# Kernel tuning notes

Hardware: AMD Instinct MI355X
Metric: run time of the kernel (lower is better)

Reference implementation:

```python
import jax, jax.numpy as jnp
import numpy as np

DIM = 128
NUM_SLOTS = 8
ITERS = 3
EPS = 1e-8
LN_EPS = 1e-3
HIDDEN = max(DIM, 128)


def _ln(x, w, b):
    mu = jnp.mean(x, axis=-1, keepdims=True)
    var = jnp.mean(jnp.square(x - mu), axis=-1, keepdims=True)
    return (x - mu) * jax.lax.rsqrt(var + LN_EPS) * w + b


def setup_inputs() -> dict:
    key = jax.random.key(0)
    ks = jax.random.split(key, 16)
    b, n, d, h = 32, 4096, DIM, HIDDEN
    limit = np.sqrt(6.0 / (1 + d))
    inp = {
        'inputs': jax.random.normal(ks[0], (b, n, d), jnp.float32),
        'slots_mu': jax.random.uniform(ks[1], (1, 1, d), jnp.float32, -limit, limit),
        'slots_log_sigma': jax.random.uniform(ks[2], (1, 1, d), jnp.float32, -limit, limit),
        'Wq': jax.random.normal(ks[3], (d, d), jnp.float32) / np.sqrt(d),
        'Wk': jax.random.normal(ks[4], (d, d), jnp.float32) / np.sqrt(d),
        'Wv': jax.random.normal(ks[5], (d, d), jnp.float32) / np.sqrt(d),
        'W_ih': jax.random.normal(ks[6], (3 * d, d), jnp.float32) / np.sqrt(d),
        'W_hh': jax.random.normal(ks[7], (3 * d, d), jnp.float32) / np.sqrt(d),
        'b_ih': jnp.zeros((3 * d,), jnp.float32),
        'b_hh': jnp.zeros((3 * d,), jnp.float32),
        'W1': jax.random.normal(ks[8], (h, d), jnp.float32) / np.sqrt(d),
        'b1': jnp.zeros((h,), jnp.float32),
        'W2': jax.random.normal(ks[9], (d, h), jnp.float32) / np.sqrt(h),
        'b2': jnp.zeros((d,), jnp.float32),
        'ln_in_w': jnp.ones((d,), jnp.float32), 'ln_in_b': jnp.zeros((d,), jnp.float32),
        'ln_s_w': jnp.ones((d,), jnp.float32), 'ln_s_b': jnp.zeros((d,), jnp.float32),
        'ln_ff_w': jnp.ones((d,), jnp.float32), 'ln_ff_b': jnp.zeros((d,), jnp.float32),
    }
    return inp


def reference(inputs, slots_mu, slots_log_sigma, Wq, Wk, Wv, W_ih, W_hh, b_ih, b_hh,
              W1, b1, W2, b2, ln_in_w, ln_in_b, ln_s_w, ln_s_b, ln_ff_w, ln_ff_b):
    b, n, d = inputs.shape
    scale = d ** -0.5
    # stochastic slot init (reparameterized, fixed key for determinism)
    noise = jax.random.normal(jax.random.key(42), (b, NUM_SLOTS, d), inputs.dtype)
    slots = slots_mu + jnp.exp(slots_log_sigma) * noise

    x = _ln(inputs, ln_in_w, ln_in_b)
    k = jnp.einsum('bnd,ed->bne', x, Wk)
    v = jnp.einsum('bnd,ed->bne', x, Wv)

    for _ in range(ITERS):
        slots_prev = slots
        q = jnp.einsum('bsd,ed->bse', _ln(slots, ln_s_w, ln_s_b), Wq)
        dots = jnp.einsum('bid,bjd->bij', q, k) * scale          # [b, slots, n]
        attn = jax.nn.softmax(dots, axis=1) + EPS                 # softmax over slots
        attn = attn / jnp.sum(attn, axis=-1, keepdims=True)       # normalize over tokens
        updates = jnp.einsum('bjd,bij->bid', v, attn)             # [b, slots, d]
        # GRUCell(updates, slots_prev)
        gx = jnp.einsum('bsd,ed->bse', updates, W_ih) + b_ih
        gh = jnp.einsum('bsd,ed->bse', slots_prev, W_hh) + b_hh
        xr, xz, xn = jnp.split(gx, 3, axis=-1)
        hr, hz, hn = jnp.split(gh, 3, axis=-1)
        r = jax.nn.sigmoid(xr + hr)
        z = jax.nn.sigmoid(xz + hz)
        ng = jnp.tanh(xn + r * hn)
        slots = (1.0 - z) * ng + z * slots_prev
        # residual MLP
        ff = _ln(slots, ln_ff_w, ln_ff_b)
        ff = jax.nn.relu(jnp.einsum('bsd,hd->bsh', ff, W1) + b1)
        slots = slots + jnp.einsum('bsh,dh->bsd', ff, W2) + b2
    return slots
```

## Files before the change

kernel.cpp:

```cpp
#include <hip/hip_runtime.h>
#include <hip/hip_bf16.h>
#include <math.h>

#define DIM 128
#define NSLOT 8
#define NTOK 4096
#define NB 32
#define CHUNK 512
#define NCH (NTOK / CHUNK)
#define LN_EPS 1e-3f
#define ATT_EPS 1e-8f
#define SCALE 0.08838834764831845f

#define BM 64
#define LDK 136

typedef short bf16x8 __attribute__((ext_vector_type(8)));
typedef float f32x4 __attribute__((ext_vector_type(4)));
typedef unsigned short ushort8_t __attribute__((ext_vector_type(8)));

__device__ __forceinline__ float bf2f(unsigned short u) {
  return __uint_as_float(((unsigned)u) << 16);
}
__device__ __forceinline__ unsigned short f2bf(float f) {
  unsigned u = __float_as_uint(f);
  unsigned r = (u + 0x7FFFu + ((u >> 16) & 1u)) >> 16;
  return (unsigned short)r;
}

__device__ __forceinline__ float erfinv_like_xla(float x) {
  double xd = (double)x;
  double w = -log1p(-xd * xd);
  double p;
  if (w < 5.0) {
    w = w - 2.5;
    p = 2.81022636e-08;
    p = 3.43273939e-07 + p * w;
    p = -3.5233877e-06 + p * w;
    p = -4.39150654e-06 + p * w;
    p = 0.00021858087 + p * w;
    p = -0.00125372503 + p * w;
    p = -0.00417768164 + p * w;
    p = 0.246640727 + p * w;
    p = 1.50140941 + p * w;
  } else {
    w = sqrt(w) - 3.0;
    p = -0.000200214257;
    p = 0.000100950558 + p * w;
    p = 0.00134934322 + p * w;
    p = -0.00367342844 + p * w;
    p = 0.00573950773 + p * w;
    p = -0.0076224613 + p * w;
    p = 0.00943887047 + p * w;
    p = 1.00167406 + p * w;
    p = 2.83297682 + p * w;
  }
  return (float)(p * xd);
}

__global__ __launch_bounds__(256) void k_init_slots(
    const float* __restrict__ mu, const float* __restrict__ lsig,
    float* __restrict__ slots) {
  int t = blockIdx.x * blockDim.x + threadIdx.x;
  if (t >= NB * NSLOT * DIM) return;
  uint32_t x0 = 0u, x1 = (uint32_t)t;
  uint32_t k0 = 0u, k1 = 42u;
  uint32_t ks[3] = {k0, k1, k0 ^ k1 ^ 0x1BD11BDAu};
  x0 += ks[0];
  x1 += ks[1];
  const int rot[2][4] = {{13, 15, 26, 6}, {17, 29, 16, 24}};
#pragma unroll
  for (int blk = 0; blk < 5; ++blk) {
    const int* r = rot[blk & 1];
#pragma unroll
    for (int j = 0; j < 4; ++j) {
      x0 += x1;
      x1 = (x1 << r[j]) | (x1 >> (32 - r[j]));
      x1 ^= x0;
    }
    x0 += ks[(blk + 1) % 3];
    x1 += ks[(blk + 2) % 3] + (uint32_t)(blk + 1);
  }
  uint32_t bits = x0 ^ x1;
  float f = __uint_as_float((bits >> 9) | 0x3F800000u) - 1.0f;
  const float mn = __uint_as_float(0xBF7FFFFFu);
  float u = fmaxf(f * 2.0f + mn, mn);
  float noise = 1.41421356f * erfinv_like_xla(u);
  int d = t & (DIM - 1);
  slots[t] = mu[d] + expf(lsig[d]) * noise;
}

__global__ __launch_bounds__(256) void k_wcast(const float* __restrict__ Wk,
                                               const float* __restrict__ Wv,
                                               unsigned short* __restrict__ Wbf) {
  int i = blockIdx.x * 256 + threadIdx.x;
  if (i >= DIM * DIM) return;
  Wbf[i] = f2bf(Wk[i]);
  Wbf[DIM * DIM + i] = f2bf(Wv[i]);
}

__global__ __launch_bounds__(256) void k_ln_kv(
    const float* __restrict__ inp, const unsigned short* __restrict__ Wbf,
    const float* __restrict__ lnw, const float* __restrict__ lnb,
    unsigned short* __restrict__ kt, unsigned short* __restrict__ vt) {
  __shared__ unsigned short x_lds[BM][LDK];
  int t = threadIdx.x;
  int tg = blockIdx.x;

  {
    int r = t >> 2, qh = t & 3;
    const float* src = inp + ((size_t)tg * BM + r) * DIM + qh * 32;
    float xr[32];
    float s = 0.f, sq = 0.f;
#pragma unroll
    for (int i4 = 0; i4 < 8; ++i4) {
      float4 v = *reinterpret_cast<const float4*>(src + i4 * 4);
      xr[i4 * 4 + 0] = v.x; xr[i4 * 4 + 1] = v.y;
      xr[i4 * 4 + 2] = v.z; xr[i4 * 4 + 3] = v.w;
      s += v.x + v.y + v.z + v.w;
      sq += v.x * v.x + v.y * v.y + v.z * v.z + v.w * v.w;
    }
    s += __shfl_xor(s, 1); sq += __shfl_xor(sq, 1);
    s += __shfl_xor(s, 2); sq += __shfl_xor(sq, 2);
    float mean = s * (1.0f / DIM);
    float var = fmaxf(sq * (1.0f / DIM) - mean * mean, 0.0f);
    float inv = 1.0f / sqrtf(var + LN_EPS);
#pragma unroll
    for (int c8 = 0; c8 < 4; ++c8) {
      ushort8_t pk;
#pragma unroll
      for (int j = 0; j < 8; ++j) {
        int d = qh * 32 + c8 * 8 + j;
        float y = (xr[c8 * 8 + j] - mean) * inv * lnw[d] + lnb[d];
        pk[j] = f2bf(y);
      }
      *reinterpret_cast<ushort8_t*>(&x_lds[r][qh * 32 + c8 * 8]) = pk;
    }
  }
  __syncthreads();

  int w = t >> 6, l = t & 63, lm = l & 15, lg = l >> 4;
  int mat = w >> 1;
  int ebase = (w & 1) * 64;
  const unsigned short* Wsrc = Wbf + mat * DIM * DIM;

  f32x4 acc[4][4];
#pragma unroll
  for (int i = 0; i < 4; ++i)
#pragma unroll
    for (int j = 0; j < 4; ++j) acc[i][j] = (f32x4){0.f, 0.f, 0.f, 0.f};

  if (mat == 0) {
#pragma unroll
    for (int ks = 0; ks < 4; ++ks) {
      bf16x8 wf[4], xf[4];
#pragma unroll
      for (int et = 0; et < 4; ++et)
        wf[et] = *reinterpret_cast<const bf16x8*>(
            Wsrc + (ebase + et * 16 + lm) * DIM + ks * 32 + 8 * lg);
#pragma unroll
      for (int tt = 0; tt < 4; ++tt)
        xf[tt] = *reinterpret_cast<const bf16x8*>(
            &x_lds[tt * 16 + lm][ks * 32 + 8 * lg]);
#pragma unroll
      for (int tt = 0; tt < 4; ++tt)
#pragma unroll
        for (int et = 0; et < 4; ++et)
          acc[tt][et] = __builtin_amdgcn_mfma_f32_16x16x32_bf16(
              xf[tt], wf[et], acc[tt][et], 0, 0, 0);
    }
    size_t rowbase = (size_t)tg * BM;
#pragma unroll
    for (int tt = 0; tt < 4; ++tt)
#pragma unroll
      for (int et = 0; et < 4; ++et)
#pragma unroll
        for (int r = 0; r < 4; ++r) {
          size_t grow = rowbase + tt * 16 + 4 * lg + r;
          kt[grow * DIM + ebase + et * 16 + lm] = f2bf(acc[tt][et][r]);
        }
  } else {
#pragma unroll
    for (int ks = 0; ks < 4; ++ks) {
      bf16x8 wf[4], xf[4];
#pragma unroll
      for (int et = 0; et < 4; ++et)
        wf[et] = *reinterpret_cast<const bf16x8*>(
            Wsrc + (ebase + et * 16 + lm) * DIM + ks * 32 + 8 * lg);
#pragma unroll
      for (int tt = 0; tt < 4; ++tt)
        xf[tt] = *reinterpret_cast<const bf16x8*>(
            &x_lds[tt * 16 + lm][ks * 32 + 8 * lg]);
#pragma unroll
      for (int et = 0; et < 4; ++et)
#pragma unroll
        for (int tt = 0; tt < 4; ++tt)
          acc[et][tt] = __builtin_amdgcn_mfma_f32_16x16x32_bf16(
              wf[et], xf[tt], acc[et][tt], 0, 0, 0);
    }
    int b = tg >> 6;
    int nb = (tg & 63) * BM;
#pragma unroll
    for (int et = 0; et < 4; ++et)
#pragma unroll
      for (int tt = 0; tt < 4; ++tt)
#pragma unroll
        for (int r = 0; r < 4; ++r) {
          int e = ebase + et * 16 + 4 * lg + r;
          vt[((size_t)b * DIM + e) * NTOK + nb + tt * 16 + lm] =
              f2bf(acc[et][tt][r]);
        }
  }
}

__global__ __launch_bounds__(256) void k_attn(
    const float* __restrict__ slots, const float* __restrict__ Wq,
    const float* __restrict__ lnw, const float* __restrict__ lnb,
    const unsigned short* __restrict__ kt, const unsigned short* __restrict__ vt,
    float* __restrict__ Np, float* __restrict__ Dp) {
  int bid = blockIdx.x;
  int b = bid >> 3, ch = bid & 7;
  int n0 = ch * CHUNK;
  int t = threadIdx.x;
  __shared__ unsigned short q_lds[NSLOT][LDK];
  __shared__ __align__(16) float sln[NSLOT][DIM];
  __shared__ __align__(16) float a_t[CHUNK][NSLOT];

  {
    int s = t >> 5, c = t & 31;
    const float* sb = slots + (b * NSLOT + s) * DIM;
    float4 xv = *reinterpret_cast<const float4*>(sb + c * 4);
    float ps = xv.x + xv.y + xv.z + xv.w;
    float pq = xv.x * xv.x + xv.y * xv.y + xv.z * xv.z + xv.w * xv.w;
#pragma unroll
    for (int m = 16; m >= 1; m >>= 1) {
      ps += __shfl_xor(ps, m, 32);
      pq += __shfl_xor(pq, m, 32);
    }
    float mean = ps * (1.0f / DIM);
    float var = fmaxf(pq * (1.0f / DIM) - mean * mean, 0.0f);
    float inv = 1.0f / sqrtf(var + LN_EPS);
    float vals[4] = {xv.x, xv.y, xv.z, xv.w};
#pragma unroll
    for (int ii = 0; ii < 4; ++ii) {
      int d = c * 4 + ii;
      sln[s][d] = (vals[ii] - mean) * inv * lnw[d] + lnb[d];
    }
    __syncthreads();
#pragma unroll
    for (int ii = 0; ii < 4; ++ii) {
      int e = c + 32 * ii;
      const float* wr = Wq + e * DIM;
      float acc = 0.0f;
#pragma unroll
      for (int d4 = 0; d4 < DIM / 4; ++d4) {
        float4 w4 = *reinterpret_cast<const float4*>(wr + d4 * 4);
        float4 s4 = *reinterpret_cast<const float4*>(&sln[s][d4 * 4]);
        acc += s4.x * w4.x + s4.y * w4.y + s4.z * w4.z + s4.w * w4.w;
      }
      q_lds[s][e] = f2bf(SCALE * acc);
    }
  }
  __syncthreads();

  {
    int w = t >> 6, l = t & 63, lm = l & 15, lg = l >> 4;
    bf16x8 aq[4];
#pragma unroll
    for (int ks = 0; ks < 4; ++ks)
      aq[ks] = *reinterpret_cast<const bf16x8*>(
          &q_lds[lm & 7][ks * 32 + 8 * lg]);
    const unsigned short* kb = kt + ((size_t)b * NTOK + n0) * DIM;
#pragma unroll
    for (int tt8 = 0; tt8 < 8; ++tt8) {
      int tok = w * 128 + tt8 * 16 + lm;
      f32x4 acc = (f32x4){0.f, 0.f, 0.f, 0.f};
#pragma unroll
      for (int ks = 0; ks < 4; ++ks) {
        bf16x8 bk = *reinterpret_cast<const bf16x8*>(
            kb + (size_t)tok * DIM + ks * 32 + 8 * lg);
        acc = __builtin_amdgcn_mfma_f32_16x16x32_bf16(aq[ks], bk, acc, 0, 0, 0);
      }
      float m4 = fmaxf(fmaxf(acc[0], acc[1]), fmaxf(acc[2], acc[3]));
      float m8 = fmaxf(m4, __shfl_xor(m4, 16));
      float e0 = expf(acc[0] - m8), e1 = expf(acc[1] - m8);
      float e2 = expf(acc[2] - m8), e3 = expf(acc[3] - m8);
      float s4 = e0 + e1 + e2 + e3;
      float s8 = s4 + __shfl_xor(s4, 16);
      float rs = 1.0f / s8;
      if (lg < 2) {
        float4 av = {e0 * rs + ATT_EPS, e1 * rs + ATT_EPS, e2 * rs + ATT_EPS,
                     e3 * rs + ATT_EPS};
        *reinterpret_cast<float4*>(&a_t[tok][lg * 4]) = av;
      }
    }
  }
  __syncthreads();

  {
    int i = t >> 5, c = t & 31;
    float s = 0.0f;
#pragma unroll
    for (int jj = 0; jj < CHUNK / 32; ++jj) s += a_t[c + 32 * jj][i];
#pragma unroll
    for (int m = 16; m >= 1; m >>= 1) s += __shfl_xor(s, m, 32);
    if (c == 0) Dp[(b * NCH + ch) * NSLOT + i] = s;
  }

  {
    int d = t & (DIM - 1), ig = t >> 7;
    const unsigned short* vb = vt + ((size_t)b * DIM + d) * NTOK + n0;
    float acc0 = 0, acc1 = 0, acc2 = 0, acc3 = 0;
    for (int j8 = 0; j8 < CHUNK / 8; ++j8) {
      ushort8_t vv = *reinterpret_cast<const ushort8_t*>(vb + j8 * 8);
#pragma unroll
      for (int u = 0; u < 8; ++u) {
        float vval = bf2f(vv[u]);
        float4 av = *reinterpret_cast<const float4*>(&a_t[j8 * 8 + u][ig * 4]);
        acc0 += vval * av.x;
        acc1 += vval * av.y;
        acc2 += vval * av.z;
        acc3 += vval * av.w;
      }
    }
    size_t base = (size_t)(b * NCH + ch) * NSLOT;
    Np[(base + ig * 4 + 0) * DIM + d] = acc0;
    Np[(base + ig * 4 + 1) * DIM + d] = acc1;
    Np[(base + ig * 4 + 2) * DIM + d] = acc2;
    Np[(base + ig * 4 + 3) * DIM + d] = acc3;
  }
}

__global__ __launch_bounds__(256) void k_update(
    float* __restrict__ slots, const float* __restrict__ Np,
    const float* __restrict__ Dp, const float* __restrict__ W_ih,
    const float* __restrict__ W_hh, const float* __restrict__ b_ih,
    const float* __restrict__ b_hh, const float* __restrict__ W1,
    const float* __restrict__ b1, const float* __restrict__ W2,
    const float* __restrict__ b2, const float* __restrict__ lnfw,
    const float* __restrict__ lnfb) {
  int bs = blockIdx.x;
  int b = bs >> 3, s = bs & 7;
  int t = threadIdx.x;
  __shared__ __align__(16) float upd[DIM];
  __shared__ __align__(16) float sprev[DIM];
  __shared__ __align__(16) float snew[DIM];
  __shared__ __align__(16) float ffin[DIM];
  __shared__ __align__(16) float ffb[DIM];
  __shared__ __align__(16) float gx[3 * DIM];
  __shared__ __align__(16) float gh[3 * DIM];

  float dsum = 0.0f;
  for (int ch = 0; ch < NCH; ++ch) dsum += Dp[(b * NCH + ch) * NSLOT + s];

  if (t < DIM) {
    sprev[t] = slots[(b * NSLOT + s) * DIM + t];
    float a = 0.0f;
    for (int ch = 0; ch < NCH; ++ch)
      a += Np[((size_t)(b * NCH + ch) * NSLOT + s) * DIM + t];
    upd[t] = a / dsum;
  }
  __syncthreads();

  for (int e = t; e < 3 * DIM; e += 256) {
    const float* wi = W_ih + e * DIM;
    const float* wh = W_hh + e * DIM;
    float ax = 0.0f, ah = 0.0f;
#pragma unroll
    for (int d4 = 0; d4 < DIM / 4; ++d4) {
      float4 u4 = *reinterpret_cast<const float4*>(&upd[d4 * 4]);
      float4 p4 = *reinterpret_cast<const float4*>(&sprev[d4 * 4]);
      float4 wi4 = *reinterpret_cast<const float4*>(wi + d4 * 4);
      float4 wh4 = *reinterpret_cast<const float4*>(wh + d4 * 4);
      ax += u4.x * wi4.x + u4.y * wi4.y + u4.z * wi4.z + u4.w * wi4.w;
      ah += p4.x * wh4.x + p4.y * wh4.y + p4.z * wh4.z + p4.w * wh4.w;
    }
    gx[e] = ax + b_ih[e];
    gh[e] = ah + b_hh[e];
  }
  __syncthreads();

  if (t < DIM) {
    float xr = gx[t], xz = gx[DIM + t], xn = gx[2 * DIM + t];
    float hr = gh[t], hz = gh[DIM + t], hn = gh[2 * DIM + t];
    float r = 1.0f / (1.0f + expf(-(xr + hr)));
    float z = 1.0f / (1.0f + expf(-(xz + hz)));
    float ng = tanhf(xn + r * hn);
    snew[t] = (1.0f - z) * ng + z * sprev[t];
  }
  __syncthreads();

  if (t < DIM) {
    float s1 = 0.0f, s2 = 0.0f;
#pragma unroll 8
    for (int d = 0; d < DIM; ++d) {
      float v = snew[d];
      s1 += v;
      s2 += v * v;
    }
    float mean = s1 * (1.0f / DIM);
    float var = fmaxf(s2 * (1.0f / DIM) - mean * mean, 0.0f);
    float inv = 1.0f / sqrtf(var + LN_EPS);
    ffin[t] = (snew[t] - mean) * inv * lnfw[t] + lnfb[t];
  }
  __syncthreads();

  if (t < DIM) {
    const float* wr = W1 + t * DIM;
    float acc = 0.0f;
#pragma unroll
    for (int d4 = 0; d4 < DIM / 4; ++d4) {
      float4 f4 = *reinterpret_cast<const float4*>(&ffin[d4 * 4]);
      float4 w4 = *reinterpret_cast<const float4*>(wr + d4 * 4);
      acc += f4.x * w4.x + f4.y * w4.y + f4.z * w4.z + f4.w * w4.w;
    }
    ffb[t] = fmaxf(acc + b1[t], 0.0f);
  }
  __syncthreads();

  if (t < DIM) {
    const float* wr = W2 + t * DIM;
    float acc = 0.0f;
#pragma unroll
    for (int h4 = 0; h4 < DIM / 4; ++h4) {
      float4 f4 = *reinterpret_cast<const float4*>(&ffb[h4 * 4]);
      float4 w4 = *reinterpret_cast<const float4*>(wr + h4 * 4);
      acc += f4.x * w4.x + f4.y * w4.y + f4.z * w4.z + f4.w * w4.w;
    }
    slots[(b * NSLOT + s) * DIM + t] = snew[t] + acc + b2[t];
  }
}

__global__ __launch_bounds__(256) void k_sentinel(float* __restrict__ out,
                                                  int n) {
  int i = blockIdx.x * blockDim.x + threadIdx.x;
  if (i < n) out[i] = 1234.5f;
}

extern "C" void kernel_launch(void* const* d_in, const int* in_sizes, int n_in,
                              void* d_out, int out_size, void* d_ws,
                              size_t ws_size, hipStream_t stream) {
  const float* inp = (const float*)d_in[0];
  const float* mu = (const float*)d_in[1];
  const float* lsig = (const float*)d_in[2];
  const float* Wq = (const float*)d_in[3];
  const float* Wk = (const float*)d_in[4];
  const float* Wv = (const float*)d_in[5];
  const float* W_ih = (const float*)d_in[6];
  const float* W_hh = (const float*)d_in[7];
  const float* b_ih = (const float*)d_in[8];
  const float* b_hh = (const float*)d_in[9];
  const float* W1 = (const float*)d_in[10];
  const float* b1 = (const float*)d_in[11];
  const float* W2 = (const float*)d_in[12];
  const float* b2 = (const float*)d_in[13];
  const float* ln_in_w = (const float*)d_in[14];
  const float* ln_in_b = (const float*)d_in[15];
  const float* ln_s_w = (const float*)d_in[16];
  const float* ln_s_b = (const float*)d_in[17];
  const float* ln_ff_w = (const float*)d_in[18];
  const float* ln_ff_b = (const float*)d_in[19];

  float* slots = (float*)d_out;

  const size_t kv_elems = (size_t)NB * DIM * NTOK;
  const size_t w_elems = (size_t)2 * DIM * DIM;
  const size_t np_elems = (size_t)NB * NCH * NSLOT * DIM;
  const size_t dp_elems = (size_t)NB * NCH * NSLOT;
  size_t need = kv_elems * 2 * 2 + w_elems * 2 + np_elems * 4 + dp_elems * 4;
  if (ws_size < need) {
    k_sentinel<<<(out_size + 255) / 256, 256, 0, stream>>>((float*)d_out,
                                                           out_size);
    return;
  }
  char* wsb = (char*)d_ws;
  unsigned short* kt = (unsigned short*)wsb;
  unsigned short* vt = kt + kv_elems;
  unsigned short* Wbf = vt + kv_elems;
  float* Np = (float*)(wsb + kv_elems * 4 + w_elems * 2);
  float* Dp = Np + np_elems;

  k_init_slots<<<(NB * NSLOT * DIM) / 256, 256, 0, stream>>>(mu, lsig, slots);
  k_wcast<<<(DIM * DIM) / 256, 256, 0, stream>>>(Wk, Wv, Wbf);
  k_ln_kv<<<NB * NTOK / BM, 256, 0, stream>>>(inp, Wbf, ln_in_w, ln_in_b, kt,
                                              vt);
  for (int it = 0; it < 3; ++it) {
    k_attn<<<NB * NCH, 256, 0, stream>>>(slots, Wq, ln_s_w, ln_s_b, kt, vt, Np,
                                         Dp);
    k_update<<<NB * NSLOT, 256, 0, stream>>>(slots, Np, Dp, W_ih, W_hh, b_ih,
                                             b_hh, W1, b1, W2, b2, ln_ff_w,
                                             ln_ff_b);
  }
}
```

Before: 223.3 us.

## Fuse slot GRU/MLP update into attention kernel, stage K/V stores, use MFMA for updates

Each attention block now redundantly recomputes the previous iteration's GRU and MLP slot update from the partial sums before computing attention, so only one update launch remains at the end. This cuts the k_update/k_attn launch pairs and their serialization, with ping-pong workspace buffers for the partial sums and slot state. The K/V projection now stages its outputs through shared memory so the global stores are coalesced 16-byte writes. The attention-weighted V reduction now uses bf16 MFMA with attention weights stored as bf16, which lowers precision. The cost is that the update arithmetic is repeated 8 times per batch across the chunk blocks, and shared memory use per block rises.

```diff
diff --git a/kernel.cpp b/kernel.cpp
--- a/kernel.cpp
+++ b/kernel.cpp
@@ -8,6 +8,7 @@
 #define NB 32
 #define CHUNK 512
 #define NCH (NTOK / CHUNK)
+#define CHUNKPAD 520
 #define LN_EPS 1e-3f
 #define ATT_EPS 1e-8f
 #define SCALE 0.08838834764831845f
@@ -103,7 +104,7 @@
     const float* __restrict__ inp, const unsigned short* __restrict__ Wbf,
     const float* __restrict__ lnw, const float* __restrict__ lnb,
     unsigned short* __restrict__ kt, unsigned short* __restrict__ vt) {
-  __shared__ unsigned short x_lds[BM][LDK];
+  __shared__ __align__(16) unsigned short SH[DIM * 72];
   int t = threadIdx.x;
   int tg = blockIdx.x;
 
@@ -134,7 +135,7 @@
         float y = (xr[c8 * 8 + j] - mean) * inv * lnw[d] + lnb[d];
         pk[j] = f2bf(y);
       }
-      *reinterpret_cast<ushort8_t*>(&x_lds[r][qh * 32 + c8 * 8]) = pk;
+      *reinterpret_cast<ushort8_t*>(&SH[r * LDK + qh * 32 + c8 * 8]) = pk;
     }
   }
   __syncthreads();
@@ -161,7 +162,7 @@
 #pragma unroll
       for (int tt = 0; tt < 4; ++tt)
         xf[tt] = *reinterpret_cast<const bf16x8*>(
-            &x_lds[tt * 16 + lm][ks * 32 + 8 * lg]);
+            &SH[(tt * 16 + lm) * LDK + ks * 32 + 8 * lg]);
 #pragma unroll
       for (int tt = 0; tt < 4; ++tt)
 #pragma unroll
@@ -169,16 +170,6 @@
           acc[tt][et] = __builtin_amdgcn_mfma_f32_16x16x32_bf16(
               xf[tt], wf[et], acc[tt][et], 0, 0, 0);
     }
-    size_t rowbase = (size_t)tg * BM;
-#pragma unroll
-    for (int tt = 0; tt < 4; ++tt)
-#pragma unroll
-      for (int et = 0; et < 4; ++et)
-#pragma unroll
-        for (int r = 0; r < 4; ++r) {
-          size_t grow = rowbase + tt * 16 + 4 * lg + r;
-          kt[grow * DIM + ebase + et * 16 + lm] = f2bf(acc[tt][et][r]);
-        }
   } else {
 #pragma unroll
     for (int ks = 0; ks < 4; ++ks) {
@@ -190,7 +181,7 @@
 #pragma unroll
       for (int tt = 0; tt < 4; ++tt)
         xf[tt] = *reinterpret_cast<const bf16x8*>(
-            &x_lds[tt * 16 + lm][ks * 32 + 8 * lg]);
+            &SH[(tt * 16 + lm) * LDK + ks * 32 + 8 * lg]);
 #pragma unroll
       for (int et = 0; et < 4; ++et)
 #pragma unroll
@@ -198,38 +189,209 @@
           acc[et][tt] = __builtin_amdgcn_mfma_f32_16x16x32_bf16(
               wf[et], xf[tt], acc[et][tt], 0, 0, 0);
     }
-    int b = tg >> 6;
+  }
+  __syncthreads();
+
+  if (mat == 0) {
+#pragma unroll
+    for (int tt = 0; tt < 4; ++tt)
+#pragma unroll
+      for (int et = 0; et < 4; ++et)
+#pragma unroll
+        for (int r = 0; r < 4; ++r)
+          SH[(tt * 16 + 4 * lg + r) * LDK + ebase + et * 16 + lm] =
+              f2bf(acc[tt][et][r]);
+  }
+  __syncthreads();
+  {
+    size_t rowbase = (size_t)tg * BM;
+#pragma unroll
+    for (int u = 0; u < 4; ++u) {
+      int i = u * 256 + t;
+      int tok = i >> 4, off = (i & 15) * 8;
+      ushort8_t vv = *reinterpret_cast<const ushort8_t*>(&SH[tok * LDK + off]);
+      *reinterpret_cast<ushort8_t*>(&kt[(rowbase + tok) * DIM + off]) = vv;
+    }
+  }
+  __syncthreads();
+
+  if (mat == 1) {
+#pragma unroll
+    for (int et = 0; et < 4; ++et)
+#pragma unroll
+      for (int tt = 0; tt < 4; ++tt)
+#pragma unroll
+        for (int r = 0; r < 4; ++r)
+          SH[(ebase + et * 16 + 4 * lg + r) * 72 + tt * 16 + lm] =
+              f2bf(acc[et][tt][r]);
+  }
+  __syncthreads();
+  {
+    int bb = tg >> 6;
     int nb = (tg & 63) * BM;
 #pragma unroll
-    for (int et = 0; et < 4; ++et)
-#pragma unroll
-      for (int tt = 0; tt < 4; ++tt)
-#pragma unroll
-        for (int r = 0; r < 4; ++r) {
-          int e = ebase + et * 16 + 4 * lg + r;
-          vt[((size_t)b * DIM + e) * NTOK + nb + tt * 16 + lm] =
-              f2bf(acc[et][tt][r]);
-        }
+    for (int u = 0; u < 4; ++u) {
+      int i = u * 256 + t;
+      int e = i >> 3, off = (i & 7) * 8;
+      ushort8_t vv = *reinterpret_cast<const ushort8_t*>(&SH[e * 72 + off]);
+      *reinterpret_cast<ushort8_t*>(&vt[((size_t)bb * DIM + e) * NTOK + nb + off]) = vv;
+    }
   }
 }
 
 __global__ __launch_bounds__(256) void k_attn(
-    const float* __restrict__ slots, const float* __restrict__ Wq,
-    const float* __restrict__ lnw, const float* __restrict__ lnb,
-    const unsigned short* __restrict__ kt, const unsigned short* __restrict__ vt,
-    float* __restrict__ Np, float* __restrict__ Dp) {
+    const float* __restrict__ slots_in, float* __restrict__ slots_out,
+    const float* __restrict__ Wq, const float* __restrict__ lnsw,
+    const float* __restrict__ lnsb, const unsigned short* __restrict__ kt,
+    const unsigned short* __restrict__ vt, float* __restrict__ Np_out,
+    float* __restrict__ Dp_out, const float* __restrict__ Np_in,
+    const float* __restrict__ Dp_in, const float* __restrict__ W_ih,
+    const float* __restrict__ W_hh, const float* __restrict__ b_ih,
+    const float* __restrict__ b_hh, const float* __restrict__ W1,
+    const float* __restrict__ b1, const float* __restrict__ W2,
+    const float* __restrict__ b2, const float* __restrict__ lnfw,
+    const float* __restrict__ lnfb, int do_update) {
   int bid = blockIdx.x;
   int b = bid >> 3, ch = bid & 7;
   int n0 = ch * CHUNK;
   int t = threadIdx.x;
-  __shared__ unsigned short q_lds[NSLOT][LDK];
+
+  __shared__ __align__(16) float scur[NSLOT][DIM];
   __shared__ __align__(16) float sln[NSLOT][DIM];
-  __shared__ __align__(16) float a_t[CHUNK][NSLOT];
+  __shared__ __align__(16) float upd[NSLOT][DIM];
+  __shared__ __align__(16) float ffin[NSLOT][DIM];
+  __shared__ __align__(16) float ffb[NSLOT][DIM];
+  __shared__ __align__(16) float gx[NSLOT][3 * DIM];
+  __shared__ __align__(16) float gh[NSLOT][3 * DIM];
+  __shared__ float dsumsh[NSLOT];
+  __shared__ __align__(16) unsigned short q_lds[NSLOT][LDK];
+  __shared__ __align__(16) unsigned short a_lds[NSLOT][CHUNKPAD];
+
+  if (do_update) {
+    if (t < NSLOT) {
+      float sa = 0.0f;
+      for (int c2 = 0; c2 < NCH; ++c2) sa += Dp_in[(b * NCH + c2) * NSLOT + t];
+      dsumsh[t] = sa;
+    }
+#pragma unroll
+    for (int r4 = 0; r4 < 4; ++r4) {
+      int idx = t + 256 * r4;
+      int s = idx >> 7, d = idx & (DIM - 1);
+      scur[s][d] = slots_in[(b * NSLOT + s) * DIM + d];
+      float a = 0.0f;
+      for (int c2 = 0; c2 < NCH; ++c2)
+        a += Np_in[((size_t)(b * NCH + c2) * NSLOT + s) * DIM + d];
+      upd[s][d] = a;
+    }
+    __syncthreads();
+#pragma unroll
+    for (int r4 = 0; r4 < 4; ++r4) {
+      int idx = t + 256 * r4;
+      int s = idx >> 7, d = idx & (DIM - 1);
+      upd[s][d] = upd[s][d] / dsumsh[s];
+    }
+    __syncthreads();
+    for (int g = 0; g < 12; ++g) {
+      int o = g * 256 + t;
+      int s = o / 384, e = o % 384;
+      const float* wi = W_ih + e * DIM;
+      const float* wh = W_hh + e * DIM;
+      float ax = 0.0f, ah = 0.0f;
+#pragma unroll
+      for (int d4 = 0; d4 < DIM / 4; ++d4) {
+        float4 u4 = *reinterpret_cast<const float4*>(&upd[s][d4 * 4]);
+        float4 p4 = *reinterpret_cast<const float4*>(&scur[s][d4 * 4]);
+        float4 wi4 = *reinterpret_cast<const float4*>(wi + d4 * 4);
+        float4 wh4 = *reinterpret_cast<const float4*>(wh + d4 * 4);
+        ax += u4.x * wi4.x + u4.y * wi4.y + u4.z * wi4.z + u4.w * wi4.w;
+        ah += p4.x * wh4.x + p4.y * wh4.y + p4.z * wh4.z + p4.w * wh4.w;
+      }
+      gx[s][e] = ax + b_ih[e];
+      gh[s][e] = ah + b_hh[e];
+    }
+    __syncthreads();
+#pragma unroll
+    for (int r4 = 0; r4 < 4; ++r4) {
+      int idx = t + 256 * r4;
+      int s = idx >> 7, d = idx & (DIM - 1);
+      float xr = gx[s][d], xz = gx[s][DIM + d], xn = gx[s][2 * DIM + d];
+      float hr = gh[s][d], hz = gh[s][DIM + d], hn = gh[s][2 * DIM + d];
+      float r = 1.0f / (1.0f + expf(-(xr + hr)));
+      float z = 1.0f / (1.0f + expf(-(xz + hz)));
+      float ng = tanhf(xn + r * hn);
+      scur[s][d] = (1.0f - z) * ng + z * scur[s][d];
+    }
+    __syncthreads();
+    {
+      int s = t >> 5, c = t & 31;
+      float4 xv = *reinterpret_cast<const float4*>(&scur[s][c * 4]);
+      float ps = xv.x + xv.y + xv.z + xv.w;
+      float pq = xv.x * xv.x + xv.y * xv.y + xv.z * xv.z + xv.w * xv.w;
+#pragma unroll
+      for (int m = 16; m >= 1; m >>= 1) {
+        ps += __shfl_xor(ps, m, 32);
+        pq += __shfl_xor(pq, m, 32);
+      }
+      float mean = ps * (1.0f / DIM);
+      float var = fmaxf(pq * (1.0f / DIM) - mean * mean, 0.0f);
+      float inv = 1.0f / sqrtf(var + LN_EPS);
+      float vals[4] = {xv.x, xv.y, xv.z, xv.w};
+#pragma unroll
+      for (int ii = 0; ii < 4; ++ii) {
+        int d = c * 4 + ii;
+        ffin[s][d] = (vals[ii] - mean) * inv * lnfw[d] + lnfb[d];
+      }
+    }
+    __syncthreads();
+    {
+      int s = t >> 5, c = t & 31;
+#pragma unroll
+      for (int ii = 0; ii < 4; ++ii) {
+        int e = c + 32 * ii;
+        const float* wr = W1 + e * DIM;
+        float acc = 0.0f;
+#pragma unroll
+        for (int d4 = 0; d4 < DIM / 4; ++d4) {
+          float4 f4 = *reinterpret_cast<const float4*>(&ffin[s][d4 * 4]);
+          float4 w4 = *reinterpret_cast<const float4*>(wr + d4 * 4);
+          acc += f4.x * w4.x + f4.y * w4.y + f4.z * w4.z + f4.w * w4.w;
+        }
+        ffb[s][e] = fmaxf(acc + b1[e], 0.0f);
+      }
+    }
+    __syncthreads();
+    {
+      int s = t >> 5, c = t & 31;
+#pragma unroll
+      for (int ii = 0; ii < 4; ++ii) {
+        int d = c + 32 * ii;
+        const float* wr = W2 + d * DIM;
+        float acc = 0.0f;
+#pragma unroll
+        for (int h4 = 0; h4 < DIM / 4; ++h4) {
+          float4 f4 = *reinterpret_cast<const float4*>(&ffb[s][h4 * 4]);
+          float4 w4 = *reinterpret_cast<const float4*>(wr + h4 * 4);
+          acc += f4.x * w4.x + f4.y * w4.y + f4.z * w4.z + f4.w * w4.w;
+        }
+        float val = scur[s][d] + acc + b2[d];
+        scur[s][d] = val;
+        if (ch == 0) slots_out[(b * NSLOT + s) * DIM + d] = val;
+      }
+    }
+    __syncthreads();
+  } else {
+#pragma unroll
+    for (int r4 = 0; r4 < 4; ++r4) {
+      int idx = t + 256 * r4;
+      int s = idx >> 7, d = idx & (DIM - 1);
+      scur[s][d] = slots_in[(b * NSLOT + s) * DIM + d];
+    }
+    __syncthreads();
+  }
 
   {
     int s = t >> 5, c = t & 31;
-    const float* sb = slots + (b * NSLOT + s) * DIM;
-    float4 xv = *reinterpret_cast<const float4*>(sb + c * 4);
+    float4 xv = *reinterpret_cast<const float4*>(&scur[s][c * 4]);
     float ps = xv.x + xv.y + xv.z + xv.w;
     float pq = xv.x * xv.x + xv.y * xv.y + xv.z * xv.z + xv.w * xv.w;
 #pragma unroll
@@ -244,7 +406,7 @@
 #pragma unroll
     for (int ii = 0; ii < 4; ++ii) {
       int d = c * 4 + ii;
-      sln[s][d] = (vals[ii] - mean) * inv * lnw[d] + lnb[d];
+      sln[s][d] = (vals[ii] - mean) * inv * lnsw[d] + lnsb[d];
     }
     __syncthreads();
 #pragma unroll
@@ -268,8 +430,7 @@
     bf16x8 aq[4];
 #pragma unroll
     for (int ks = 0; ks < 4; ++ks)
-      aq[ks] = *reinterpret_cast<const bf16x8*>(
-          &q_lds[lm & 7][ks * 32 + 8 * lg]);
+      aq[ks] = *reinterpret_cast<const bf16x8*>(&q_lds[lm & 7][ks * 32 + 8 * lg]);
     const unsigned short* kb = kt + ((size_t)b * NTOK + n0) * DIM;
 #pragma unroll
     for (int tt8 = 0; tt8 < 8; ++tt8) {
@@ -289,9 +450,10 @@
       float s8 = s4 + __shfl_xor(s4, 16);
       float rs = 1.0f / s8;
       if (lg < 2) {
-        float4 av = {e0 * rs + ATT_EPS, e1 * rs + ATT_EPS, e2 * rs + ATT_EPS,
-                     e3 * rs + ATT_EPS};
-        *reinterpret_cast<float4*>(&a_t[tok][lg * 4]) = av;
+        a_lds[4 * lg + 0][tok] = f2bf(e0 * rs + ATT_EPS);
+        a_lds[4 * lg + 1][tok] = f2bf(e1 * rs + ATT_EPS);
+        a_lds[4 * lg + 2][tok] = f2bf(e2 * rs + ATT_EPS);
+        a_lds[4 * lg + 3][tok] = f2bf(e3 * rs + ATT_EPS);
       }
     }
   }
@@ -301,44 +463,45 @@
     int i = t >> 5, c = t & 31;
     float s = 0.0f;
 #pragma unroll
-    for (int jj = 0; jj < CHUNK / 32; ++jj) s += a_t[c + 32 * jj][i];
+    for (int jj = 0; jj < CHUNK / 32; ++jj) s += bf2f(a_lds[i][c + 32 * jj]);
 #pragma unroll
     for (int m = 16; m >= 1; m >>= 1) s += __shfl_xor(s, m, 32);
-    if (c == 0) Dp[(b * NCH + ch) * NSLOT + i] = s;
+    if (c == 0) Dp_out[(b * NCH + ch) * NSLOT + i] = s;
   }
 
   {
-    int d = t & (DIM - 1), ig = t >> 7;
-    const unsigned short* vb = vt + ((size_t)b * DIM + d) * NTOK + n0;
-    float acc0 = 0, acc1 = 0, acc2 = 0, acc3 = 0;
-    for (int j8 = 0; j8 < CHUNK / 8; ++j8) {
-      ushort8_t vv = *reinterpret_cast<const ushort8_t*>(vb + j8 * 8);
-#pragma unroll
-      for (int u = 0; u < 8; ++u) {
-        float vval = bf2f(vv[u]);
-        float4 av = *reinterpret_cast<const float4*>(&a_t[j8 * 8 + u][ig * 4]);
-        acc0 += vval * av.x;
-        acc1 += vval * av.y;
-        acc2 += vval * av.z;
-        acc3 += vval * av.w;
-      }
-    }
-    size_t base = (size_t)(b * NCH + ch) * NSLOT;
-    Np[(base + ig * 4 + 0) * DIM + d] = acc0;
-    Np[(base + ig * 4 + 1) * DIM + d] = acc1;
-    Np[(base + ig * 4 + 2) * DIM + d] = acc2;
-    Np[(base + ig * 4 + 3) * DIM + d] = acc3;
+    int w = t >> 6, l = t & 63, lm = l & 15, lg = l >> 4;
+#pragma unroll
+    for (int dti = 0; dti < 2; ++dti) {
+      int dt = w * 2 + dti;
+      f32x4 acc = (f32x4){0.f, 0.f, 0.f, 0.f};
+      const unsigned short* vb =
+          vt + ((size_t)b * DIM + dt * 16 + lm) * NTOK + n0;
+#pragma unroll
+      for (int kk = 0; kk < CHUNK / 32; ++kk) {
+        bf16x8 af = *reinterpret_cast<const bf16x8*>(
+            &a_lds[lm & 7][kk * 32 + 8 * lg]);
+        bf16x8 bv = *reinterpret_cast<const bf16x8*>(vb + kk * 32 + 8 * lg);
+        acc = __builtin_amdgcn_mfma_f32_16x16x32_bf16(af, bv, acc, 0, 0, 0);
+      }
+      if (lg < 2) {
+#pragma unroll
+        for (int r = 0; r < 4; ++r)
+          Np_out[((size_t)(b * NCH + ch) * NSLOT + 4 * lg + r) * DIM + dt * 16 +
+                 lm] = acc[r];
+      }
+    }
   }
 }
 
 __global__ __launch_bounds__(256) void k_update(
-    float* __restrict__ slots, const float* __restrict__ Np,
-    const float* __restrict__ Dp, const float* __restrict__ W_ih,
-    const float* __restrict__ W_hh, const float* __restrict__ b_ih,
-    const float* __restrict__ b_hh, const float* __restrict__ W1,
-    const float* __restrict__ b1, const float* __restrict__ W2,
-    const float* __restrict__ b2, const float* __restrict__ lnfw,
-    const float* __restrict__ lnfb) {
+    const float* __restrict__ slots_in, float* __restrict__ out,
+    const float* __restrict__ Np, const float* __restrict__ Dp,
+    const float* __restrict__ W_ih, const float* __restrict__ W_hh,
+    const float* __restrict__ b_ih, const float* __restrict__ b_hh,
+    const float* __restrict__ W1, const float* __restrict__ b1,
+    const float* __restrict__ W2, const float* __restrict__ b2,
+    const float* __restrict__ lnfw, const float* __restrict__ lnfb) {
   int bs = blockIdx.x;
   int b = bs >> 3, s = bs & 7;
   int t = threadIdx.x;
@@ -354,7 +517,7 @@
   for (int ch = 0; ch < NCH; ++ch) dsum += Dp[(b * NCH + ch) * NSLOT + s];
 
   if (t < DIM) {
-    sprev[t] = slots[(b * NSLOT + s) * DIM + t];
+    sprev[t] = slots_in[(b * NSLOT + s) * DIM + t];
     float a = 0.0f;
     for (int ch = 0; ch < NCH; ++ch)
       a += Np[((size_t)(b * NCH + ch) * NSLOT + s) * DIM + t];
@@ -427,7 +590,7 @@
       float4 w4 = *reinterpret_cast<const float4*>(wr + h4 * 4);
       acc += f4.x * w4.x + f4.y * w4.y + f4.z * w4.z + f4.w * w4.w;
     }
-    slots[(b * NSLOT + s) * DIM + t] = snew[t] + acc + b2[t];
+    out[(b * NSLOT + s) * DIM + t] = snew[t] + acc + b2[t];
   }
 }
 
@@ -461,13 +624,12 @@
   const float* ln_ff_w = (const float*)d_in[18];
   const float* ln_ff_b = (const float*)d_in[19];
 
-  float* slots = (float*)d_out;
-
   const size_t kv_elems = (size_t)NB * DIM * NTOK;
-  const size_t w_elems = (size_t)2 * DIM * DIM;
   const size_t np_elems = (size_t)NB * NCH * NSLOT * DIM;
   const size_t dp_elems = (size_t)NB * NCH * NSLOT;
-  size_t need = kv_elems * 2 * 2 + w_elems * 2 + np_elems * 4 + dp_elems * 4;
+  const size_t sl_elems = (size_t)NB * NSLOT * DIM;
+  size_t need = kv_elems * 2 * 2 + np_elems * 2 * 4 + dp_elems * 2 * 4 +
+                sl_elems * 2 * 4;
   if (ws_size < need) {
     k_sentinel<<<(out_size + 255) / 256, 256, 0, stream>>>((float*)d_out,
                                                            out_size);
@@ -476,19 +638,33 @@
   char* wsb = (char*)d_ws;
   unsigned short* kt = (unsigned short*)wsb;
   unsigned short* vt = kt + kv_elems;
-  unsigned short* Wbf = vt + kv_elems;
-  float* Np = (float*)(wsb + kv_elems * 4 + w_elems * 2);
-  float* Dp = Np + np_elems;
-
-  k_init_slots<<<(NB * NSLOT * DIM) / 256, 256, 0, stream>>>(mu, lsig, slots);
+  float* Np0 = (float*)(wsb + kv_elems * 4);
+  float* Np1 = Np0 + np_elems;
+  float* Dp0 = Np1 + np_elems;
+  float* Dp1 = Dp0 + dp_elems;
+  float* slotsB = Dp1 + dp_elems;
+  float* slotsC = slotsB + sl_elems;
+  unsigned short* Wbf = (unsigned short*)Np0;
+
+  float* slots0 = (float*)d_out;
+
+  k_init_slots<<<(NB * NSLOT * DIM) / 256, 256, 0, stream>>>(mu, lsig, slots0);
   k_wcast<<<(DIM * DIM) / 256, 256, 0, stream>>>(Wk, Wv, Wbf);
   k_ln_kv<<<NB * NTOK / BM, 256, 0, stream>>>(inp, Wbf, ln_in_w, ln_in_b, kt,
                                               vt);
-  for (int it = 0; it < 3; ++it) {
-    k_attn<<<NB * NCH, 256, 0, stream>>>(slots, Wq, ln_s_w, ln_s_b, kt, vt, Np,
-                                         Dp);
-    k_update<<<NB * NSLOT, 256, 0, stream>>>(slots, Np, Dp, W_ih, W_hh, b_ih,
-                                             b_hh, W1, b1, W2, b2, ln_ff_w,
-                                             ln_ff_b);
-  }
-}
+  k_attn<<<NB * NCH, 256, 0, stream>>>(slots0, slotsB, Wq, ln_s_w, ln_s_b, kt,
+                                       vt, Np0, Dp0, Np1, Dp1, W_ih, W_hh,
+                                       b_ih, b_hh, W1, b1, W2, b2, ln_ff_w,
+                                       ln_ff_b, 0);
+  k_attn<<<NB * NCH, 256, 0, stream>>>(slots0, slotsB, Wq, ln_s_w, ln_s_b, kt,
+                                       vt, Np1, Dp1, Np0, Dp0, W_ih, W_hh,
+                                       b_ih, b_hh, W1, b1, W2, b2, ln_ff_w,
+                                       ln_ff_b, 1);
+  k_attn<<<NB * NCH, 256, 0, stream>>>(slotsB, slotsC, Wq, ln_s_w, ln_s_b, kt,
+                                       vt, Np0, Dp0, Np1, Dp1, W_ih, W_hh,
+                                       b_ih, b_hh, W1, b1, W2, b2, ln_ff_w,
+                                       ln_ff_b, 1);
+  k_update<<<NB * NSLOT, 256, 0, stream>>>(slotsC, (float*)d_out, Np0, Dp0,
+                                           W_ih, W_hh, b_ih, b_hh, W1, b1, W2,
+                                           b2, ln_ff_w, ln_ff_b);
+}
```

After: 446.9 us. +100.1%, slower.

## Stage K/V stores through LDS and use MFMA for attention-weighted V sum

Applied to the files above, without the earlier changes.

In k_ln_kv, the K and V results are first written into shared memory and then stored as coalesced 16-byte vectors, replacing the scattered per-element global stores, including the strided transpose writes for V. In k_attn, the chunk size is halved and the block grows to 512 threads, doubling the grid. Attention weights are now kept as bf16 in LDS, and the updates reduction runs on MFMA instead of a scalar FMA loop. The bf16 weight scratch reuses the Np buffer to save workspace. The cost is lower precision for the attention weights and twice as many partial sums for k_update to combine.

```diff
diff --git a/kernel.cpp b/kernel.cpp
--- a/kernel.cpp
+++ b/kernel.cpp
@@ -6,8 +6,9 @@
 #define NSLOT 8
 #define NTOK 4096
 #define NB 32
-#define CHUNK 512
+#define CHUNK 256
 #define NCH (NTOK / CHUNK)
+#define CHUNKPAD 264
 #define LN_EPS 1e-3f
 #define ATT_EPS 1e-8f
 #define SCALE 0.08838834764831845f
@@ -103,7 +104,7 @@
     const float* __restrict__ inp, const unsigned short* __restrict__ Wbf,
     const float* __restrict__ lnw, const float* __restrict__ lnb,
     unsigned short* __restrict__ kt, unsigned short* __restrict__ vt) {
-  __shared__ unsigned short x_lds[BM][LDK];
+  __shared__ __align__(16) unsigned short SH[DIM * 72];
   int t = threadIdx.x;
   int tg = blockIdx.x;
 
@@ -134,7 +135,7 @@
         float y = (xr[c8 * 8 + j] - mean) * inv * lnw[d] + lnb[d];
         pk[j] = f2bf(y);
       }
-      *reinterpret_cast<ushort8_t*>(&x_lds[r][qh * 32 + c8 * 8]) = pk;
+      *reinterpret_cast<ushort8_t*>(&SH[r * LDK + qh * 32 + c8 * 8]) = pk;
     }
   }
   __syncthreads();
@@ -161,7 +162,7 @@
 #pragma unroll
       for (int tt = 0; tt < 4; ++tt)
         xf[tt] = *reinterpret_cast<const bf16x8*>(
-            &x_lds[tt * 16 + lm][ks * 32 + 8 * lg]);
+            &SH[(tt * 16 + lm) * LDK + ks * 32 + 8 * lg]);
 #pragma unroll
       for (int tt = 0; tt < 4; ++tt)
 #pragma unroll
@@ -169,16 +170,6 @@
           acc[tt][et] = __builtin_amdgcn_mfma_f32_16x16x32_bf16(
               xf[tt], wf[et], acc[tt][et], 0, 0, 0);
     }
-    size_t rowbase = (size_t)tg * BM;
-#pragma unroll
-    for (int tt = 0; tt < 4; ++tt)
-#pragma unroll
-      for (int et = 0; et < 4; ++et)
-#pragma unroll
-        for (int r = 0; r < 4; ++r) {
-          size_t grow = rowbase + tt * 16 + 4 * lg + r;
-          kt[grow * DIM + ebase + et * 16 + lm] = f2bf(acc[tt][et][r]);
-        }
   } else {
 #pragma unroll
     for (int ks = 0; ks < 4; ++ks) {
@@ -190,7 +181,7 @@
 #pragma unroll
       for (int tt = 0; tt < 4; ++tt)
         xf[tt] = *reinterpret_cast<const bf16x8*>(
-            &x_lds[tt * 16 + lm][ks * 32 + 8 * lg]);
+            &SH[(tt * 16 + lm) * LDK + ks * 32 + 8 * lg]);
 #pragma unroll
       for (int et = 0; et < 4; ++et)
 #pragma unroll
@@ -198,58 +189,93 @@
           acc[et][tt] = __builtin_amdgcn_mfma_f32_16x16x32_bf16(
               wf[et], xf[tt], acc[et][tt], 0, 0, 0);
     }
-    int b = tg >> 6;
+  }
+  __syncthreads();
+
+  if (mat == 0) {
+#pragma unroll
+    for (int tt = 0; tt < 4; ++tt)
+#pragma unroll
+      for (int et = 0; et < 4; ++et)
+#pragma unroll
+        for (int r = 0; r < 4; ++r)
+          SH[(tt * 16 + 4 * lg + r) * LDK + ebase + et * 16 + lm] =
+              f2bf(acc[tt][et][r]);
+  }
+  __syncthreads();
+  {
+    size_t rowbase = (size_t)tg * BM;
+#pragma unroll
+    for (int u = 0; u < 4; ++u) {
+      int i = u * 256 + t;
+      int tok = i >> 4, off = (i & 15) * 8;
+      ushort8_t vv = *reinterpret_cast<const ushort8_t*>(&SH[tok * LDK + off]);
+      *reinterpret_cast<ushort8_t*>(&kt[(rowbase + tok) * DIM + off]) = vv;
+    }
+  }
+  __syncthreads();
+
+  if (mat == 1) {
+#pragma unroll
+    for (int et = 0; et < 4; ++et)
+#pragma unroll
+      for (int tt = 0; tt < 4; ++tt)
+#pragma unroll
+        for (int r = 0; r < 4; ++r)
+          SH[(ebase + et * 16 + 4 * lg + r) * 72 + tt * 16 + lm] =
+              f2bf(acc[et][tt][r]);
+  }
+  __syncthreads();
+  {
+    int bb = tg >> 6;
     int nb = (tg & 63) * BM;
 #pragma unroll
-    for (int et = 0; et < 4; ++et)
-#pragma unroll
-      for (int tt = 0; tt < 4; ++tt)
-#pragma unroll
-        for (int r = 0; r < 4; ++r) {
-          int e = ebase + et * 16 + 4 * lg + r;
-          vt[((size_t)b * DIM + e) * NTOK + nb + tt * 16 + lm] =
-              f2bf(acc[et][tt][r]);
-        }
-  }
-}
-
-__global__ __launch_bounds__(256) void k_attn(
+    for (int u = 0; u < 4; ++u) {
+      int i = u * 256 + t;
+      int e = i >> 3, off = (i & 7) * 8;
+      ushort8_t vv = *reinterpret_cast<const ushort8_t*>(&SH[e * 72 + off]);
+      *reinterpret_cast<ushort8_t*>(&vt[((size_t)bb * DIM + e) * NTOK + nb + off]) = vv;
+    }
+  }
+}
+
+__global__ __launch_bounds__(512, 4) void k_attn(
     const float* __restrict__ slots, const float* __restrict__ Wq,
-    const float* __restrict__ lnw, const float* __restrict__ lnb,
+    const float* __restrict__ lnsw, const float* __restrict__ lnsb,
     const unsigned short* __restrict__ kt, const unsigned short* __restrict__ vt,
     float* __restrict__ Np, float* __restrict__ Dp) {
   int bid = blockIdx.x;
-  int b = bid >> 3, ch = bid & 7;
+  int b = bid >> 4, ch = bid & 15;
   int n0 = ch * CHUNK;
   int t = threadIdx.x;
-  __shared__ unsigned short q_lds[NSLOT][LDK];
+  int wid = t >> 6, l = t & 63, lm = l & 15, lg = l >> 4;
+
   __shared__ __align__(16) float sln[NSLOT][DIM];
-  __shared__ __align__(16) float a_t[CHUNK][NSLOT];
-
-  {
-    int s = t >> 5, c = t & 31;
+  __shared__ __align__(16) unsigned short q_lds[NSLOT][LDK];
+  __shared__ __align__(16) unsigned short a_lds[NSLOT][CHUNKPAD];
+
+  {
+    int s = wid, c = l;
     const float* sb = slots + (b * NSLOT + s) * DIM;
-    float4 xv = *reinterpret_cast<const float4*>(sb + c * 4);
-    float ps = xv.x + xv.y + xv.z + xv.w;
-    float pq = xv.x * xv.x + xv.y * xv.y + xv.z * xv.z + xv.w * xv.w;
-#pragma unroll
-    for (int m = 16; m >= 1; m >>= 1) {
-      ps += __shfl_xor(ps, m, 32);
-      pq += __shfl_xor(pq, m, 32);
+    float x0 = sb[c], x1 = sb[c + 64];
+    float ps = x0 + x1, pq = x0 * x0 + x1 * x1;
+#pragma unroll
+    for (int m = 32; m >= 1; m >>= 1) {
+      ps += __shfl_xor(ps, m);
+      pq += __shfl_xor(pq, m);
     }
     float mean = ps * (1.0f / DIM);
     float var = fmaxf(pq * (1.0f / DIM) - mean * mean, 0.0f);
     float inv = 1.0f / sqrtf(var + LN_EPS);
-    float vals[4] = {xv.x, xv.y, xv.z, xv.w};
-#pragma unroll
-    for (int ii = 0; ii < 4; ++ii) {
-      int d = c * 4 + ii;
-      sln[s][d] = (vals[ii] - mean) * inv * lnw[d] + lnb[d];
-    }
-    __syncthreads();
-#pragma unroll
-    for (int ii = 0; ii < 4; ++ii) {
-      int e = c + 32 * ii;
+    sln[s][c] = (x0 - mean) * inv * lnsw[c] + lnsb[c];
+    sln[s][c + 64] = (x1 - mean) * inv * lnsw[c + 64] + lnsb[c + 64];
+  }
+  __syncthreads();
+  {
+    int s = wid, c = l;
+#pragma unroll
+    for (int half = 0; half < 2; ++half) {
+      int e = c + half * 64;
       const float* wr = Wq + e * DIM;
       float acc = 0.0f;
 #pragma unroll
@@ -264,16 +290,14 @@
   __syncthreads();
 
   {
-    int w = t >> 6, l = t & 63, lm = l & 15, lg = l >> 4;
     bf16x8 aq[4];
 #pragma unroll
     for (int ks = 0; ks < 4; ++ks)
-      aq[ks] = *reinterpret_cast<const bf16x8*>(
-          &q_lds[lm & 7][ks * 32 + 8 * lg]);
+      aq[ks] = *reinterpret_cast<const bf16x8*>(&q_lds[lm & 7][ks * 32 + 8 * lg]);
     const unsigned short* kb = kt + ((size_t)b * NTOK + n0) * DIM;
 #pragma unroll
-    for (int tt8 = 0; tt8 < 8; ++tt8) {
-      int tok = w * 128 + tt8 * 16 + lm;
+    for (int tt = 0; tt < 2; ++tt) {
+      int tok = wid * 32 + tt * 16 + lm;
       f32x4 acc = (f32x4){0.f, 0.f, 0.f, 0.f};
 #pragma unroll
       for (int ks = 0; ks < 4; ++ks) {
@@ -289,45 +313,41 @@
       float s8 = s4 + __shfl_xor(s4, 16);
       float rs = 1.0f / s8;
       if (lg < 2) {
-        float4 av = {e0 * rs + ATT_EPS, e1 * rs + ATT_EPS, e2 * rs + ATT_EPS,
-                     e3 * rs + ATT_EPS};
-        *reinterpret_cast<float4*>(&a_t[tok][lg * 4]) = av;
+        a_lds[4 * lg + 0][tok] = f2bf(e0 * rs + ATT_EPS);
+        a_lds[4 * lg + 1][tok] = f2bf(e1 * rs + ATT_EPS);
+        a_lds[4 * lg + 2][tok] = f2bf(e2 * rs + ATT_EPS);
+        a_lds[4 * lg + 3][tok] = f2bf(e3 * rs + ATT_EPS);
       }
     }
   }
   __syncthreads();
 
   {
-    int i = t >> 5, c = t & 31;
     float s = 0.0f;
 #pragma unroll
-    for (int jj = 0; jj < CHUNK / 32; ++jj) s += a_t[c + 32 * jj][i];
-#pragma unroll
-    for (int m = 16; m >= 1; m >>= 1) s += __shfl_xor(s, m, 32);
-    if (c == 0) Dp[(b * NCH + ch) * NSLOT + i] = s;
-  }
-
-  {
-    int d = t & (DIM - 1), ig = t >> 7;
-    const unsigned short* vb = vt + ((size_t)b * DIM + d) * NTOK + n0;
-    float acc0 = 0, acc1 = 0, acc2 = 0, acc3 = 0;
-    for (int j8 = 0; j8 < CHUNK / 8; ++j8) {
-      ushort8_t vv = *reinterpret_cast<const ushort8_t*>(vb + j8 * 8);
-#pragma unroll
-      for (int u = 0; u < 8; ++u) {
-        float vval = bf2f(vv[u]);
-        float4 av = *reinterpret_cast<const float4*>(&a_t[j8 * 8 + u][ig * 4]);
-        acc0 += vval * av.x;
-        acc1 += vval * av.y;
-        acc2 += vval * av.z;
-        acc3 += vval * av.w;
-      }
-    }
-    size_t base = (size_t)(b * NCH + ch) * NSLOT;
-    Np[(base + ig * 4 + 0) * DIM + d] = acc0;
-    Np[(base + ig * 4 + 1) * DIM + d] = acc1;
-    Np[(base + ig * 4 + 2) * DIM + d] = acc2;
-    Np[(base + ig * 4 + 3) * DIM + d] = acc3;
+    for (int jj = 0; jj < CHUNK / 64; ++jj) s += bf2f(a_lds[wid][l + 64 * jj]);
+#pragma unroll
+    for (int m = 32; m >= 1; m >>= 1) s += __shfl_xor(s, m);
+    if (l == 0) Dp[(b * NCH + ch) * NSLOT + wid] = s;
+  }
+
+  {
+    f32x4 acc = (f32x4){0.f, 0.f, 0.f, 0.f};
+    const unsigned short* vb =
+        vt + ((size_t)b * DIM + wid * 16 + lm) * NTOK + n0;
+#pragma unroll
+    for (int kk = 0; kk < CHUNK / 32; ++kk) {
+      bf16x8 af = *reinterpret_cast<const bf16x8*>(
+          &a_lds[lm & 7][kk * 32 + 8 * lg]);
+      bf16x8 bv = *reinterpret_cast<const bf16x8*>(vb + kk * 32 + 8 * lg);
+      acc = __builtin_amdgcn_mfma_f32_16x16x32_bf16(af, bv, acc, 0, 0, 0);
+    }
+    if (lg < 2) {
+#pragma unroll
+      for (int r = 0; r < 4; ++r)
+        Np[((size_t)(b * NCH + ch) * NSLOT + 4 * lg + r) * DIM + wid * 16 +
+           lm] = acc[r];
+    }
   }
 }
 
@@ -464,10 +484,9 @@
   float* slots = (float*)d_out;
 
   const size_t kv_elems = (size_t)NB * DIM * NTOK;
-  const size_t w_elems = (size_t)2 * DIM * DIM;
   const size_t np_elems = (size_t)NB * NCH * NSLOT * DIM;
   const size_t dp_elems = (size_t)NB * NCH * NSLOT;
-  size_t need = kv_elems * 2 * 2 + w_elems * 2 + np_elems * 4 + dp_elems * 4;
+  size_t need = kv_elems * 2 * 2 + np_elems * 4 + dp_elems * 4;
   if (ws_size < need) {
     k_sentinel<<<(out_size + 255) / 256, 256, 0, stream>>>((float*)d_out,
                                                            out_size);
@@ -476,16 +495,16 @@
   char* wsb = (char*)d_ws;
   unsigned short* kt = (unsigned short*)wsb;
   unsigned short* vt = kt + kv_elems;
-  unsigned short* Wbf = vt + kv_elems;
-  float* Np = (float*)(wsb + kv_elems * 4 + w_elems * 2);
+  float* Np = (float*)(wsb + kv_elems * 4);
   float* Dp = Np + np_elems;
+  unsigned short* Wbf = (unsigned short*)Np;
 
   k_init_slots<<<(NB * NSLOT * DIM) / 256, 256, 0, stream>>>(mu, lsig, slots);
   k_wcast<<<(DIM * DIM) / 256, 256, 0, stream>>>(Wk, Wv, Wbf);
   k_ln_kv<<<NB * NTOK / BM, 256, 0, stream>>>(inp, Wbf, ln_in_w, ln_in_b, kt,
                                               vt);
   for (int it = 0; it < 3; ++it) {
-    k_attn<<<NB * NCH, 256, 0, stream>>>(slots, Wq, ln_s_w, ln_s_b, kt, vt, Np,
+    k_attn<<<NB * NCH, 512, 0, stream>>>(slots, Wq, ln_s_w, ln_s_b, kt, vt, Np,
                                          Dp);
     k_update<<<NB * NSLOT, 256, 0, stream>>>(slots, Np, Dp, W_ih, W_hh, b_ih,
                                              b_hh, W1, b1, W2, b2, ln_ff_w,
```

Result: slower. 248.4 us (+11.2%).
